# Kernel tuning notes

Measured on AMD Instinct MI355X. Metric: run time of the kernel, lower is better.

Reference implementation:

```python
import jax, jax.numpy as jnp
import numpy as np

N_NODES = 50000
N_EDGES = 800000
D_IN = 128
D_OUT = 128


def setup_inputs() -> dict:
    key = jax.random.key(0)
    k1, k2, k3, k4, k5 = jax.random.split(key, 5)
    x = jax.random.normal(k1, (N_NODES, D_IN), dtype=jnp.float32)
    edge_index = jax.random.randint(k2, (2, N_EDGES), 0, N_NODES, dtype=jnp.int64)
    scale = 1.0 / np.sqrt(D_IN)
    W_rel = jax.random.normal(k3, (D_OUT, D_IN), dtype=jnp.float32) * scale
    b_rel = jax.random.normal(k4, (D_OUT,), dtype=jnp.float32) * scale
    W_root = jax.random.normal(k5, (D_OUT, D_IN), dtype=jnp.float32) * scale
    return {"x": x, "edge_index": edge_index, "W_rel": W_rel, "b_rel": b_rel, "W_root": W_root}


def reference(x, edge_index, W_rel, b_rel, W_root):
    # PyG GraphConv (aggr='add'):
    #   out_i = W_rel @ (sum_{j->i} x_j) + b_rel + W_root @ x_i
    # followed by ReLU (normalization=None, dropout=0 -> identity).
    src = edge_index[0]  # message source j
    dst = edge_index[1]  # message target i
    n = x.shape[0]
    agg = jax.ops.segment_sum(x[src], dst, num_segments=n)  # [N, D_IN]
    out = agg @ W_rel.T + b_rel + x @ W_root.T              # [N, D_OUT]
    return jax.nn.relu(out)
```

## Files before the change

kernel.cpp:

```cpp
#include <hip/hip_runtime.h>
#include <hip/hip_bf16.h>


#define N_NODES 50000
#define N_EDGES 800000
#define D 128
#define SLOTS 40
#define CSTR 8
#define NPB 32
#define KC 32
#define SROW 136

#define CVT_N  (N_NODES * (D / 2))
#define PACK_N (8 * 8 * 64 * 8)
#define CNT_N  (N_NODES * CSTR + 4)

typedef __attribute__((ext_vector_type(8))) short short8;
typedef __attribute__((ext_vector_type(4))) float floatx4;

__device__ __forceinline__ float bf2f(unsigned short u) {
    return __uint_as_float((unsigned int)u << 16);
}
__device__ __forceinline__ unsigned short f2bf(float f) {
    __hip_bfloat16 h = __float2bfloat16(f);
    return *(unsigned short*)&h;
}

__device__ __forceinline__ int wave_detect_i64(const int* __restrict__ ei) {
    int lane = threadIdx.x & 63;
    int v = ei[2 * lane + 1];
    return __ballot(v == 0) == ~0ull;
}

__global__ __launch_bounds__(256) void zero_f4_kernel(float4* __restrict__ p, int n4) {
    int i = blockIdx.x * 256 + threadIdx.x;
    if (i < n4) p[i] = make_float4(0.f, 0.f, 0.f, 0.f);
}

__global__ void detect_kernel(const int* __restrict__ ei, int* __restrict__ flag) {
    if (threadIdx.x == 0 && blockIdx.x == 0) {
        int any = 0;
        for (int i = 0; i < 64; ++i) any |= ei[2 * i + 1];
        flag[0] = (any == 0) ? 1 : 0;
    }
}

__global__ __launch_bounds__(256) void prep_kernel(const float2* __restrict__ x2,
                                                   ushort2* __restrict__ xb2,
                                                   const float* __restrict__ Wrel,
                                                   const float* __restrict__ Wroot,
                                                   unsigned short* __restrict__ pwc,
                                                   int* __restrict__ cnt) {
    int i = blockIdx.x * 256 + threadIdx.x;
    if (i < CVT_N) {
        float2 f = x2[i];
        xb2[i] = make_ushort2(f2bf(f.x), f2bf(f.y));
    } else if (i < CVT_N + PACK_N) {
        int idx  = i - CVT_N;
        int j    = idx & 7;
        int lane = (idx >> 3) & 63;
        int n0   = (idx >> 9) & 7;
        int t    = idx >> 12;
        int n = n0 * 16 + (lane & 15);
        int k = t * 32 + (lane >> 4) * 8 + j;
        float w = (k < D) ? Wrel[n * D + k] : Wroot[n * D + (k - D)];
        pwc[idx] = f2bf(w);
    } else if (i < CVT_N + PACK_N + CNT_N) {
        cnt[i - CVT_N - PACK_N] = 0;
    }
}

__global__ __launch_bounds__(256) void append_kernel(const int* __restrict__ ei,
                                                     int* __restrict__ cnt,
                                                     int* __restrict__ slots,
                                                     int* __restrict__ ovf_cnt,
                                                     int* __restrict__ ovf) {
    int i64 = wave_detect_i64(ei);
    int base = (blockIdx.x * 256 + threadIdx.x) * 2;
    if (base >= N_EDGES) return;
    int s0, s1, d0, d1;
    if (i64) {
        int4 a = *(const int4*)&ei[2 * base];
        s0 = a.x; s1 = a.z;
        int4 c = *(const int4*)&ei[2 * N_EDGES + 2 * base];
        d0 = c.x; d1 = c.z;
    } else {
        int2 sv = *(const int2*)&ei[base];
        int2 dv = *(const int2*)&ei[N_EDGES + base];
        s0 = sv.x; s1 = sv.y;
        d0 = dv.x; d1 = dv.y;
    }
    bool v0 = (unsigned)s0 < N_NODES && (unsigned)d0 < N_NODES;
    bool v1 = (unsigned)s1 < N_NODES && (unsigned)d1 < N_NODES;
    int p0 = v0 ? atomicAdd(&cnt[d0 * CSTR], 1) : 0;
    int p1 = v1 ? atomicAdd(&cnt[d1 * CSTR], 1) : 0;
    if (v0) { if (p0 < SLOTS) slots[d0 * SLOTS + p0] = s0;
              else { int o = atomicAdd(ovf_cnt, 1); ovf[2 * o] = d0; ovf[2 * o + 1] = s0; } }
    if (v1) { if (p1 < SLOTS) slots[d1 * SLOTS + p1] = s1;
              else { int o = atomicAdd(ovf_cnt, 1); ovf[2 * o] = d1; ovf[2 * o + 1] = s1; } }
}

__global__ __launch_bounds__(256) void GraphConvLayer_55783035240593_kernel(
        const ushort2* __restrict__ xb2,
        const unsigned short* __restrict__ xb,
        const int* __restrict__ cnt,
        const int* __restrict__ slots,
        const int* __restrict__ ovf_cnt,
        const int* __restrict__ ovf,
        const unsigned short* __restrict__ pwc,
        const float* __restrict__ b_rel,
        float* __restrict__ out) {
    __shared__ unsigned short sA[16 * SROW];
    int wid  = threadIdx.x >> 6;
    int lane = threadIdx.x & 63;
    int node0 = blockIdx.x * 16;
    int tov = ovf_cnt[0];

    for (int li = 0; li < 4; ++li) {
        int node = node0 + wid * 4 + li;
        int kk = cnt[node * CSTR];
        if (kk > SLOTS) kk = SLOTS;
        int myidx = (lane < kk) ? slots[node * SLOTS + lane] : 0;
        float ax = 0.f, ay = 0.f;
        for (int j = 0; j < kk; j += 8) {
            int s0 = __shfl(myidx, j);
            int s1 = __shfl(myidx, j + 1);
            int s2 = __shfl(myidx, j + 2);
            int s3 = __shfl(myidx, j + 3);
            int s4 = __shfl(myidx, j + 4);
            int s5 = __shfl(myidx, j + 5);
            int s6 = __shfl(myidx, j + 6);
            int s7 = __shfl(myidx, j + 7);
            ushort2 u0 = xb2[(size_t)s0 * (D / 2) + lane];
            ushort2 u1 = xb2[(size_t)s1 * (D / 2) + lane];
            ushort2 u2 = xb2[(size_t)s2 * (D / 2) + lane];
            ushort2 u3 = xb2[(size_t)s3 * (D / 2) + lane];
            ushort2 u4 = xb2[(size_t)s4 * (D / 2) + lane];
            ushort2 u5 = xb2[(size_t)s5 * (D / 2) + lane];
            ushort2 u6 = xb2[(size_t)s6 * (D / 2) + lane];
            ushort2 u7 = xb2[(size_t)s7 * (D / 2) + lane];
            float m1 = (j + 1 < kk) ? 1.f : 0.f;
            float m2 = (j + 2 < kk) ? 1.f : 0.f;
            float m3 = (j + 3 < kk) ? 1.f : 0.f;
            float m4 = (j + 4 < kk) ? 1.f : 0.f;
            float m5 = (j + 5 < kk) ? 1.f : 0.f;
            float m6 = (j + 6 < kk) ? 1.f : 0.f;
            float m7 = (j + 7 < kk) ? 1.f : 0.f;
            ax += bf2f(u0.x) + m1 * bf2f(u1.x) + m2 * bf2f(u2.x) + m3 * bf2f(u3.x)
                + m4 * bf2f(u4.x) + m5 * bf2f(u5.x) + m6 * bf2f(u6.x) + m7 * bf2f(u7.x);
            ay += bf2f(u0.y) + m1 * bf2f(u1.y) + m2 * bf2f(u2.y) + m3 * bf2f(u3.y)
                + m4 * bf2f(u4.y) + m5 * bf2f(u5.y) + m6 * bf2f(u6.y) + m7 * bf2f(u7.y);
        }
        if (tov > 0) {
            for (int t2 = 0; t2 < tov; ++t2) {
                if (ovf[2 * t2] == node) {
                    ushort2 u = xb2[(size_t)ovf[2 * t2 + 1] * (D / 2) + lane];
                    ax += bf2f(u.x);
                    ay += bf2f(u.y);
                }
            }
        }
        *(ushort2*)&sA[(wid * 4 + li) * SROW + 2 * lane] =
            make_ushort2(f2bf(ax), f2bf(ay));
    }
    __syncthreads();

    int m = lane & 15, quad = lane >> 4;
    const unsigned short* arow = &sA[m * SROW + quad * 8];
    const unsigned short* xrow = xb + (size_t)(node0 + m) * D + quad * 8;

    floatx4 acc0 = (floatx4){0.f, 0.f, 0.f, 0.f};
    floatx4 acc1 = (floatx4){0.f, 0.f, 0.f, 0.f};
#pragma unroll
    for (int t = 0; t < 8; ++t) {
        short8 afrag = (t < 4) ? *(const short8*)(arow + t * 32)
                               : *(const short8*)(xrow + (t - 4) * 32);
        const unsigned short* bb = pwc + ((size_t)(t * 8 + wid * 2) * 64 + lane) * 8;
        short8 b0 = *(const short8*)bb;
        short8 b1 = *(const short8*)(bb + 64 * 8);
        acc0 = __builtin_amdgcn_mfma_f32_16x16x32_bf16(afrag, b0, acc0, 0, 0, 0);
        acc1 = __builtin_amdgcn_mfma_f32_16x16x32_bf16(afrag, b1, acc1, 0, 0, 0);
    }

#pragma unroll
    for (int q = 0; q < 2; ++q) {
        floatx4 a = q ? acc1 : acc0;
        int n = (wid * 2 + q) * 16 + m;
        float bias = b_rel[n];
#pragma unroll
        for (int r = 0; r < 4; ++r) {
            int node = node0 + quad * 4 + r;
            out[(size_t)node * D + n] = fmaxf(a[r] + bias, 0.f);
        }
    }
}

__global__ __launch_bounds__(256) void pack_w_kernel(const float* __restrict__ W,
                                                     float* __restrict__ pw) {
    int idx = blockIdx.x * 256 + threadIdx.x;
    if (idx >= D * D) return;
    int o = idx >> 7, k = idx & 127;
    pw[k * D + o] = W[o * D + k];
}

__global__ __launch_bounds__(256) void hist_kernel(const int* __restrict__ ei,
                                                   int* __restrict__ deg) {
    int i64 = wave_detect_i64(ei);
    int base = (blockIdx.x * 256 + threadIdx.x) * 4;
    if (base >= N_EDGES) return;
    int d0, d1, d2, d3;
    if (i64) {
        int4 a = *(const int4*)&ei[2 * N_EDGES + 2 * base];
        int4 b = *(const int4*)&ei[2 * N_EDGES + 2 * base + 4];
        d0 = a.x; d1 = a.z; d2 = b.x; d3 = b.z;
    } else {
        int4 v = *(const int4*)&ei[N_EDGES + base];
        d0 = v.x; d1 = v.y; d2 = v.z; d3 = v.w;
    }
    if ((unsigned)d0 < N_NODES) atomicAdd(&deg[d0], 1);
    if ((unsigned)d1 < N_NODES) atomicAdd(&deg[d1], 1);
    if ((unsigned)d2 < N_NODES) atomicAdd(&deg[d2], 1);
    if ((unsigned)d3 < N_NODES) atomicAdd(&deg[d3], 1);
}

__device__ __forceinline__ int wave_iscan(int v, int lane) {
#pragma unroll
    for (int off = 1; off < 64; off <<= 1) {
        int u = __shfl_up(v, off, 64);
        if (lane >= off) v += u;
    }
    return v;
}

__global__ __launch_bounds__(1024) void scan_kernel(const int* __restrict__ deg,
                                                    int* __restrict__ offsets,
                                                    int* __restrict__ cursor) {
    __shared__ int wsum[16];
    __shared__ int base_s;
    int t = threadIdx.x, lane = t & 63, w = t >> 6;
    if (t == 0) { base_s = 0; offsets[0] = 0; }
    __syncthreads();
    for (int c0 = 0; c0 < N_NODES; c0 += 1024) {
        int idx = c0 + t;
        int v = (idx < N_NODES) ? deg[idx] : 0;
        int inc = wave_iscan(v, lane);
        if (lane == 63) wsum[w] = inc;
        __syncthreads();
        if (w == 0) {
            int s = (lane < 16) ? wsum[lane] : 0;
            int si = wave_iscan(s, lane);
            if (lane < 16) wsum[lane] = si - s;
        }
        __syncthreads();
        int tot = base_s + wsum[w] + inc;
        if (idx < N_NODES) {
            offsets[idx + 1] = tot;
            cursor[idx] = tot - v;
        }
        __syncthreads();
        if (t == 1023) base_s = tot;
        __syncthreads();
    }
}

__global__ __launch_bounds__(256) void reorder_kernel(const int* __restrict__ ei,
                                                      int* __restrict__ cursor,
                                                      int* __restrict__ csr_src) {
    int i64 = wave_detect_i64(ei);
    int base = (blockIdx.x * 256 + threadIdx.x) * 4;
    if (base >= N_EDGES) return;
    int s0, s1, s2, s3, d0, d1, d2, d3;
    if (i64) {
        int4 a = *(const int4*)&ei[2 * base];
        int4 b = *(const int4*)&ei[2 * base + 4];
        s0 = a.x; s1 = a.z; s2 = b.x; s3 = b.z;
        int4 c = *(const int4*)&ei[2 * N_EDGES + 2 * base];
        int4 e = *(const int4*)&ei[2 * N_EDGES + 2 * base + 4];
        d0 = c.x; d1 = c.z; d2 = e.x; d3 = e.z;
    } else {
        int4 sv = *(const int4*)&ei[base];
        int4 dv = *(const int4*)&ei[N_EDGES + base];
        s0 = sv.x; s1 = sv.y; s2 = sv.z; s3 = sv.w;
        d0 = dv.x; d1 = dv.y; d2 = dv.z; d3 = dv.w;
    }
    bool v0 = (unsigned)s0 < N_NODES && (unsigned)d0 < N_NODES;
    bool v1 = (unsigned)s1 < N_NODES && (unsigned)d1 < N_NODES;
    bool v2 = (unsigned)s2 < N_NODES && (unsigned)d2 < N_NODES;
    bool v3 = (unsigned)s3 < N_NODES && (unsigned)d3 < N_NODES;
    int p0 = v0 ? atomicAdd(&cursor[d0], 1) : 0;
    int p1 = v1 ? atomicAdd(&cursor[d1], 1) : 0;
    int p2 = v2 ? atomicAdd(&cursor[d2], 1) : 0;
    int p3 = v3 ? atomicAdd(&cursor[d3], 1) : 0;
    if (v0) csr_src[p0] = s0;
    if (v1) csr_src[p1] = s1;
    if (v2) csr_src[p2] = s2;
    if (v3) csr_src[p3] = s3;
}

__global__ __launch_bounds__(256) void gather_kernel(const float2* __restrict__ x2,
                                                     const int* __restrict__ csr_src,
                                                     const int* __restrict__ offsets,
                                                     float2* __restrict__ agg2) {
    int node = blockIdx.x * 4 + (threadIdx.x >> 6);
    int lane = threadIdx.x & 63;
    if (node >= N_NODES) return;
    int beg = offsets[node], end = offsets[node + 1];
    float2 acc = make_float2(0.f, 0.f);
    for (int e = beg; e < end; ++e) {
        int s = csr_src[e];
        float2 f = x2[(size_t)s * (D / 2) + lane];
        acc.x += f.x;
        acc.y += f.y;
    }
    agg2[(size_t)node * (D / 2) + lane] = acc;
}

__global__ __launch_bounds__(256) void scatter_kernel(const float2* __restrict__ x2,
                                                      const int* __restrict__ ei,
                                                      const int* __restrict__ flag,
                                                      float* __restrict__ agg) {
    int wave = threadIdx.x >> 6;
    int lane = threadIdx.x & 63;
    int e = blockIdx.x * 4 + wave;
    if (e >= N_EDGES) return;
    int i64 = flag ? flag[0] : 0;
    int s, d;
    if (i64) { s = ei[2 * e]; d = ei[2 * N_EDGES + 2 * e]; }
    else     { s = ei[e];     d = ei[N_EDGES + e]; }
    if ((unsigned)s >= N_NODES || (unsigned)d >= N_NODES) return;
    float2 f = x2[(size_t)s * (D / 2) + lane];
    atomicAdd(&agg[(size_t)d * D + 2 * lane + 0], f.x);
    atomicAdd(&agg[(size_t)d * D + 2 * lane + 1], f.y);
}

__global__ __launch_bounds__(256) void gemm_f32_kernel(
        const float2* __restrict__ x2,
        const float* __restrict__ pwrel,
        const float* __restrict__ pwroot,
        const float* __restrict__ b_rel,
        float* __restrict__ out) {
    __shared__ float sWrel[KC * D];
    __shared__ float sWroot[KC * D];
    __shared__ float2 sAm[NPB * (KC / 2)];
    __shared__ float2 sXm[NPB * (KC / 2)];

    int t = threadIdx.x;
    int node0 = blockIdx.x * NPB;
    int tn = t >> 5;
    int to = t & 31;

    float acc[4][4];
#pragma unroll
    for (int a = 0; a < 4; ++a)
#pragma unroll
        for (int b = 0; b < 4; ++b) acc[a][b] = 0.0f;

    for (int c = 0; c < 4; ++c) {
        __syncthreads();
#pragma unroll
        for (int r = 0; r < 4; ++r) {
            int i = r * 256 + t;
            ((float4*)sWrel)[i]  = ((const float4*)(pwrel  + c * KC * D))[i];
            ((float4*)sWroot)[i] = ((const float4*)(pwroot + c * KC * D))[i];
        }
#pragma unroll
        for (int r = 0; r < 2; ++r) {
            int i = r * 256 + t;
            int n = i >> 4, k2 = i & 15;
            int node = node0 + n;
            float2 av = make_float2(0.f, 0.f), xv = make_float2(0.f, 0.f);
            if (node < N_NODES) {
                av = ((const float2*)out)[(size_t)node * (D / 2) + c * (KC / 2) + k2];
                xv = x2[(size_t)node * (D / 2) + c * (KC / 2) + k2];
            }
            sAm[i] = av;
            sXm[i] = xv;
        }
        __syncthreads();

#pragma unroll
        for (int k2 = 0; k2 < KC / 2; ++k2) {
            float4 wr0 = *(const float4*)&sWrel[(2 * k2 + 0) * D + to * 4];
            float4 wr1 = *(const float4*)&sWrel[(2 * k2 + 1) * D + to * 4];
            float4 wt0 = *(const float4*)&sWroot[(2 * k2 + 0) * D + to * 4];
            float4 wt1 = *(const float4*)&sWroot[(2 * k2 + 1) * D + to * 4];
#pragma unroll
            for (int ni = 0; ni < 4; ++ni) {
                float2 a  = sAm[(tn * 4 + ni) * (KC / 2) + k2];
                float2 xx = sXm[(tn * 4 + ni) * (KC / 2) + k2];
                acc[ni][0] += a.x * wr0.x + a.y * wr1.x + xx.x * wt0.x + xx.y * wt1.x;
                acc[ni][1] += a.x * wr0.y + a.y * wr1.y + xx.x * wt0.y + xx.y * wt1.y;
                acc[ni][2] += a.x * wr0.z + a.y * wr1.z + xx.x * wt0.z + xx.y * wt1.z;
                acc[ni][3] += a.x * wr0.w + a.y * wr1.w + xx.x * wt0.w + xx.y * wt1.w;
            }
        }
    }

    int o0 = to * 4;
    float4 bias = *(const float4*)&b_rel[o0];
#pragma unroll
    for (int ni = 0; ni < 4; ++ni) {
        int node = node0 + tn * 4 + ni;
        if (node >= N_NODES) continue;
        float4 v;
        v.x = fmaxf(acc[ni][0] + bias.x, 0.f);
        v.y = fmaxf(acc[ni][1] + bias.y, 0.f);
        v.z = fmaxf(acc[ni][2] + bias.z, 0.f);
        v.w = fmaxf(acc[ni][3] + bias.w, 0.f);
        *(float4*)&out[(size_t)node * D + o0] = v;
    }
}

__global__ __launch_bounds__(128) void gemm_fallback_kernel(const float* __restrict__ x,
                                                            const float* __restrict__ Wrel,
                                                            const float* __restrict__ Wroot,
                                                            const float* __restrict__ b_rel,
                                                            float* __restrict__ out) {
    __shared__ float rowA[D];
    __shared__ float rowX[D];
    int node = blockIdx.x;
    int o = threadIdx.x;
    rowA[o] = out[(size_t)node * D + o];
    rowX[o] = x[(size_t)node * D + o];
    __syncthreads();
    float acc = b_rel[o];
    const float4* wr = (const float4*)&Wrel[o * D];
    const float4* wt = (const float4*)&Wroot[o * D];
#pragma unroll 8
    for (int k4 = 0; k4 < D / 4; ++k4) {
        float4 w = wr[k4], u = wt[k4];
        const float* a = &rowA[k4 * 4];
        const float* xx = &rowX[k4 * 4];
        acc += a[0] * w.x + a[1] * w.y + a[2] * w.z + a[3] * w.w
             + xx[0] * u.x + xx[1] * u.y + xx[2] * u.z + xx[3] * u.w;
    }
    __syncthreads();
    out[(size_t)node * D + o] = fmaxf(acc, 0.f);
}

extern "C" void kernel_launch(void* const* d_in, const int* in_sizes, int n_in,
                              void* d_out, int out_size, void* d_ws, size_t ws_size,
                              hipStream_t stream) {
    const float* x      = (const float*)d_in[0];
    const int*   ei     = (const int*)d_in[1];
    const float* W_rel  = (const float*)d_in[2];
    const float* b_rel  = (const float*)d_in[3];
    const float* W_root = (const float*)d_in[4];
    float*       out    = (float*)d_out;

    char* p = (char*)d_ws;
    size_t o0 = 16;
    int*            flag    = (int*)p;
    unsigned short* pwc     = (unsigned short*)(p + o0);  o0 += (size_t)PACK_N * 2;
    unsigned short* xb      = (unsigned short*)(p + o0);  o0 += (size_t)N_NODES * D * 2;
    int*            cnt     = (int*)(p + o0);             o0 += (size_t)N_NODES * CSTR * 4;
    int*            ovf_cnt = (int*)(p + o0);             o0 += 16;
    int*            slots   = (int*)(p + o0);             o0 += (size_t)N_NODES * SLOTS * 4;
    int*            ovf     = (int*)(p + o0);             o0 += (size_t)N_EDGES * 8;
    const size_t need_full = o0;

    size_t m0 = 16;
    float* m_pwrel  = (float*)(p + m0);  m0 += (size_t)D * D * 4;
    float* m_pwroot = (float*)(p + m0);  m0 += (size_t)D * D * 4;
    int*   m_deg    = (int*)(p + m0);    m0 += (size_t)N_NODES * 4;
    int*   m_offs   = (int*)(p + m0);    m0 += ((size_t)N_NODES + 1) * 4 + 12;
    m0 &= ~15ull;
    int*   m_csr    = (int*)(p + m0);    m0 += (size_t)N_EDGES * 4;
    const size_t need_mid = m0;
    const size_t need_pw  = 16 + 2 * (size_t)D * D * 4;

    const int eb4 = (N_EDGES / 4 + 255) / 256;
    const int eb2 = (N_EDGES / 2 + 255) / 256;

    if (ws_size >= need_full) {
        const int prep_total = CVT_N + PACK_N + CNT_N;
        prep_kernel<<<(prep_total + 255) / 256, 256, 0, stream>>>(
            (const float2*)x, (ushort2*)xb, W_rel, W_root, pwc, cnt);
        append_kernel<<<eb2, 256, 0, stream>>>(ei, cnt, slots,
                                               cnt + N_NODES * CSTR, ovf);
        GraphConvLayer_55783035240593_kernel<<<N_NODES / 16, 256, 0, stream>>>(
            (const ushort2*)xb, xb, cnt, slots, cnt + N_NODES * CSTR, ovf,
            pwc, b_rel, out);
        (void)ovf_cnt;
    } else if (ws_size >= need_mid) {
        pack_w_kernel<<<64, 256, 0, stream>>>(W_rel, m_pwrel);
        pack_w_kernel<<<64, 256, 0, stream>>>(W_root, m_pwroot);
        zero_f4_kernel<<<(N_NODES / 4 + 255) / 256, 256, 0, stream>>>((float4*)m_deg,
                                                                      N_NODES / 4);
        hist_kernel<<<eb4, 256, 0, stream>>>(ei, m_deg);
        scan_kernel<<<1, 1024, 0, stream>>>(m_deg, m_offs, m_deg);
        reorder_kernel<<<eb4, 256, 0, stream>>>(ei, m_deg, m_csr);
        gather_kernel<<<N_NODES / 4, 256, 0, stream>>>((const float2*)x, m_csr,
                                                       m_offs, (float2*)out);
        gemm_f32_kernel<<<(N_NODES + NPB - 1) / NPB, 256, 0, stream>>>(
            (const float2*)x, m_pwrel, m_pwroot, b_rel, out);
    } else {
        bool have_flag = ws_size >= 16;
        bool have_pw   = ws_size >= need_pw;
        if (have_flag) detect_kernel<<<1, 64, 0, stream>>>(ei, flag);
        if (have_pw) {
            pack_w_kernel<<<64, 256, 0, stream>>>(W_rel, m_pwrel);
            pack_w_kernel<<<64, 256, 0, stream>>>(W_root, m_pwroot);
        }
        int n4 = N_NODES * D / 4;
        zero_f4_kernel<<<(n4 + 255) / 256, 256, 0, stream>>>((float4*)out, n4);
        scatter_kernel<<<N_EDGES / 4, 256, 0, stream>>>((const float2*)x, ei,
                                                        have_flag ? flag : nullptr, out);
        if (have_pw)
            gemm_f32_kernel<<<(N_NODES + NPB - 1) / NPB, 256, 0, stream>>>(
                (const float2*)x, m_pwrel, m_pwroot, b_rel, out);
        else
            gemm_fallback_kernel<<<N_NODES, 128, 0, stream>>>(x, W_rel, W_root, b_rel, out);
    }
}
```

Before: 177.2 us.

## Fuse prep, edge append and aggregation-GEMM into one persistent kernel with grid barriers

Replaces the three separate launches (prep/convert, edge append, gather+MFMA GEMM) with a single persistent kernel of 1024 blocks that uses software grid barriers between phases. It also packs the per-node counter into the slot row itself (stride 48, 47 slots plus count) and uses nontemporal stores. The intent is to cut launch overhead and inter-kernel gaps and to improve locality between count and slots. The risk is barrier spin cost, a deadlock if all 1024 blocks cannot be co-resident, and lower parallelism in the final phase because tiles are strided across a fixed grid.

Result: slower. 481.9 us (+171.9%).

```diff
diff --git a/kernel.cpp b/kernel.cpp
--- a/kernel.cpp
+++ b/kernel.cpp
@@ -5,15 +5,18 @@
 #define N_NODES 50000
 #define N_EDGES 800000
 #define D 128
-#define SLOTS 40
-#define CSTR 8
+#define NBLK 1024
+#define NTH (NBLK * 256)
+#define SLOT_STRIDE 48
+#define SLOT_CAP 47
+#define SROW 136
 #define NPB 32
 #define KC 32
-#define SROW 136
-
+
+#define EAPP   (N_EDGES / 2)
 #define CVT_N  (N_NODES * (D / 2))
 #define PACK_N (8 * 8 * 64 * 8)
-#define CNT_N  (N_NODES * CSTR + 4)
+#define PACK2_N (PACK_N / 2)
 
 typedef __attribute__((ext_vector_type(8))) short short8;
 typedef __attribute__((ext_vector_type(4))) float floatx4;
@@ -30,6 +33,191 @@
     int lane = threadIdx.x & 63;
     int v = ei[2 * lane + 1];
     return __ballot(v == 0) == ~0ull;
+}
+
+__device__ __forceinline__ void grid_barrier(int* bar, int target) {
+    __syncthreads();
+    if (threadIdx.x == 0) {
+        __threadfence();
+        atomicAdd(bar, 1);
+        while (atomicAdd(bar, 0) < target) __builtin_amdgcn_s_sleep(8);
+    }
+    __syncthreads();
+    __threadfence();
+}
+
+__global__ void init_ctl_kernel(int* __restrict__ ctl) {
+    if (threadIdx.x < 4) ctl[threadIdx.x] = 0;
+}
+
+__global__ __launch_bounds__(256, 4) void GraphConvLayer_55783035240593_kernel(
+        const float2* __restrict__ x2,
+        const int* __restrict__ ei,
+        const float* __restrict__ Wrel,
+        const float* __restrict__ Wroot,
+        const float* __restrict__ b_rel,
+        unsigned short* __restrict__ pwc,
+        unsigned short* __restrict__ xb,
+        int* __restrict__ slots,
+        int* __restrict__ ovf,
+        int* __restrict__ ctl,
+        float* __restrict__ out) {
+    __shared__ unsigned short sA[16 * SROW];
+    int tid  = threadIdx.x;
+    int gid  = blockIdx.x * 256 + tid;
+    int lane = tid & 63;
+    int wid  = tid >> 6;
+    int i64  = wave_detect_i64(ei);
+
+    for (int n = gid; n < N_NODES; n += NTH)
+        __builtin_nontemporal_store(0, &slots[n * SLOT_STRIDE]);
+
+    grid_barrier(ctl, NBLK);
+
+    const int total1 = EAPP + CVT_N + PACK2_N;
+    for (int i = gid; i < total1; i += NTH) {
+        if (i < EAPP) {
+            int base = i * 2;
+            int s0, s1, d0, d1;
+            if (i64) {
+                int4 a = *(const int4*)&ei[2 * base];
+                s0 = a.x; s1 = a.z;
+                int4 c = *(const int4*)&ei[2 * N_EDGES + 2 * base];
+                d0 = c.x; d1 = c.z;
+            } else {
+                int2 sv = *(const int2*)&ei[base];
+                int2 dv = *(const int2*)&ei[N_EDGES + base];
+                s0 = sv.x; s1 = sv.y;
+                d0 = dv.x; d1 = dv.y;
+            }
+            bool v0 = (unsigned)s0 < N_NODES && (unsigned)d0 < N_NODES;
+            bool v1 = (unsigned)s1 < N_NODES && (unsigned)d1 < N_NODES;
+            int p0 = v0 ? atomicAdd(&slots[d0 * SLOT_STRIDE], 1) : 0;
+            int p1 = v1 ? atomicAdd(&slots[d1 * SLOT_STRIDE], 1) : 0;
+            if (v0) {
+                if (p0 < SLOT_CAP)
+                    __builtin_nontemporal_store(s0, &slots[d0 * SLOT_STRIDE + 1 + p0]);
+                else {
+                    int o = atomicAdd(&ctl[1], 1);
+                    __builtin_nontemporal_store(d0, &ovf[2 * o]);
+                    __builtin_nontemporal_store(s0, &ovf[2 * o + 1]);
+                }
+            }
+            if (v1) {
+                if (p1 < SLOT_CAP)
+                    __builtin_nontemporal_store(s1, &slots[d1 * SLOT_STRIDE + 1 + p1]);
+                else {
+                    int o = atomicAdd(&ctl[1], 1);
+                    __builtin_nontemporal_store(d1, &ovf[2 * o]);
+                    __builtin_nontemporal_store(s1, &ovf[2 * o + 1]);
+                }
+            }
+        } else if (i < EAPP + CVT_N) {
+            int c = i - EAPP;
+            float2 f = x2[c];
+            unsigned int v = (unsigned int)f2bf(f.x) | ((unsigned int)f2bf(f.y) << 16);
+            __builtin_nontemporal_store(v, (unsigned int*)xb + c);
+        } else {
+            int pi = i - EAPP - CVT_N;
+            int idx  = 2 * pi;
+            int j    = idx & 7;
+            int ln   = (idx >> 3) & 63;
+            int n0   = (idx >> 9) & 7;
+            int t    = idx >> 12;
+            int n = n0 * 16 + (ln & 15);
+            int k = t * 32 + (ln >> 4) * 8 + j;
+            float w0 = (k     < D) ? Wrel[n * D + k]     : Wroot[n * D + (k - D)];
+            float w1 = (k + 1 < D) ? Wrel[n * D + k + 1] : Wroot[n * D + (k + 1 - D)];
+            unsigned int v = (unsigned int)f2bf(w0) | ((unsigned int)f2bf(w1) << 16);
+            __builtin_nontemporal_store(v, (unsigned int*)pwc + pi);
+        }
+    }
+
+    grid_barrier(ctl, 2 * NBLK);
+
+    int tov = ctl[1];
+    int m = lane & 15, quad = lane >> 4;
+
+    for (int tile = blockIdx.x; tile < N_NODES / 16; tile += NBLK) {
+        int node0 = tile * 16;
+
+        for (int li = 0; li < 4; ++li) {
+            int node = node0 + wid * 4 + li;
+            int kk = slots[node * SLOT_STRIDE];
+            if (kk > SLOT_CAP) kk = SLOT_CAP;
+            int myidx = (lane < kk) ? slots[node * SLOT_STRIDE + 1 + lane] : 0;
+            float ax = 0.f, ay = 0.f;
+            const ushort2* xb2 = (const ushort2*)xb;
+            for (int j = 0; j < kk; j += 8) {
+                int s0 = __shfl(myidx, j);
+                int s1 = __shfl(myidx, j + 1);
+                int s2 = __shfl(myidx, j + 2);
+                int s3 = __shfl(myidx, j + 3);
+                int s4 = __shfl(myidx, j + 4);
+                int s5 = __shfl(myidx, j + 5);
+                int s6 = __shfl(myidx, j + 6);
+                int s7 = __shfl(myidx, j + 7);
+                ushort2 u0 = xb2[(size_t)s0 * (D / 2) + lane];
+                ushort2 u1 = xb2[(size_t)s1 * (D / 2) + lane];
+                ushort2 u2 = xb2[(size_t)s2 * (D / 2) + lane];
+                ushort2 u3 = xb2[(size_t)s3 * (D / 2) + lane];
+                ushort2 u4 = xb2[(size_t)s4 * (D / 2) + lane];
+                ushort2 u5 = xb2[(size_t)s5 * (D / 2) + lane];
+                ushort2 u6 = xb2[(size_t)s6 * (D / 2) + lane];
+                ushort2 u7 = xb2[(size_t)s7 * (D / 2) + lane];
+                float m1 = (j + 1 < kk) ? 1.f : 0.f;
+                float m2 = (j + 2 < kk) ? 1.f : 0.f;
+                float m3 = (j + 3 < kk) ? 1.f : 0.f;
+                float m4 = (j + 4 < kk) ? 1.f : 0.f;
+                float m5 = (j + 5 < kk) ? 1.f : 0.f;
+                float m6 = (j + 6 < kk) ? 1.f : 0.f;
+                float m7 = (j + 7 < kk) ? 1.f : 0.f;
+                ax += bf2f(u0.x) + m1 * bf2f(u1.x) + m2 * bf2f(u2.x) + m3 * bf2f(u3.x)
+                    + m4 * bf2f(u4.x) + m5 * bf2f(u5.x) + m6 * bf2f(u6.x) + m7 * bf2f(u7.x);
+                ay += bf2f(u0.y) + m1 * bf2f(u1.y) + m2 * bf2f(u2.y) + m3 * bf2f(u3.y)
+                    + m4 * bf2f(u4.y) + m5 * bf2f(u5.y) + m6 * bf2f(u6.y) + m7 * bf2f(u7.y);
+            }
+            if (tov > 0) {
+                for (int t2 = 0; t2 < tov; ++t2) {
+                    if (ovf[2 * t2] == node) {
+                        ushort2 u = xb2[(size_t)ovf[2 * t2 + 1] * (D / 2) + lane];
+                        ax += bf2f(u.x);
+                        ay += bf2f(u.y);
+                    }
+                }
+            }
+            *(ushort2*)&sA[(wid * 4 + li) * SROW + 2 * lane] =
+                make_ushort2(f2bf(ax), f2bf(ay));
+        }
+        __syncthreads();
+
+        const unsigned short* arow = &sA[m * SROW + quad * 8];
+        const unsigned short* xrow = xb + (size_t)(node0 + m) * D + quad * 8;
+        floatx4 acc0 = (floatx4){0.f, 0.f, 0.f, 0.f};
+        floatx4 acc1 = (floatx4){0.f, 0.f, 0.f, 0.f};
+#pragma unroll
+        for (int t = 0; t < 8; ++t) {
+            short8 afrag = (t < 4) ? *(const short8*)(arow + t * 32)
+                                   : *(const short8*)(xrow + (t - 4) * 32);
+            const unsigned short* bb = pwc + ((size_t)(t * 8 + wid * 2) * 64 + lane) * 8;
+            short8 b0 = *(const short8*)bb;
+            short8 b1 = *(const short8*)(bb + 64 * 8);
+            acc0 = __builtin_amdgcn_mfma_f32_16x16x32_bf16(afrag, b0, acc0, 0, 0, 0);
+            acc1 = __builtin_amdgcn_mfma_f32_16x16x32_bf16(afrag, b1, acc1, 0, 0, 0);
+        }
+#pragma unroll
+        for (int q = 0; q < 2; ++q) {
+            floatx4 a = q ? acc1 : acc0;
+            int n = (wid * 2 + q) * 16 + m;
+            float bias = b_rel[n];
+#pragma unroll
+            for (int r = 0; r < 4; ++r) {
+                int node = node0 + quad * 4 + r;
+                out[(size_t)node * D + n] = fmaxf(a[r] + bias, 0.f);
+            }
+        }
+        __syncthreads();
+    }
 }
 
 __global__ __launch_bounds__(256) void zero_f4_kernel(float4* __restrict__ p, int n4) {
@@ -42,156 +230,6 @@
         int any = 0;
         for (int i = 0; i < 64; ++i) any |= ei[2 * i + 1];
         flag[0] = (any == 0) ? 1 : 0;
-    }
-}
-
-__global__ __launch_bounds__(256) void prep_kernel(const float2* __restrict__ x2,
-                                                   ushort2* __restrict__ xb2,
-                                                   const float* __restrict__ Wrel,
-                                                   const float* __restrict__ Wroot,
-                                                   unsigned short* __restrict__ pwc,
-                                                   int* __restrict__ cnt) {
-    int i = blockIdx.x * 256 + threadIdx.x;
-    if (i < CVT_N) {
-        float2 f = x2[i];
-        xb2[i] = make_ushort2(f2bf(f.x), f2bf(f.y));
-    } else if (i < CVT_N + PACK_N) {
-        int idx  = i - CVT_N;
-        int j    = idx & 7;
-        int lane = (idx >> 3) & 63;
-        int n0   = (idx >> 9) & 7;
-        int t    = idx >> 12;
-        int n = n0 * 16 + (lane & 15);
-        int k = t * 32 + (lane >> 4) * 8 + j;
-        float w = (k < D) ? Wrel[n * D + k] : Wroot[n * D + (k - D)];
-        pwc[idx] = f2bf(w);
-    } else if (i < CVT_N + PACK_N + CNT_N) {
-        cnt[i - CVT_N - PACK_N] = 0;
-    }
-}
-
-__global__ __launch_bounds__(256) void append_kernel(const int* __restrict__ ei,
-                                                     int* __restrict__ cnt,
-                                                     int* __restrict__ slots,
-                                                     int* __restrict__ ovf_cnt,
-                                                     int* __restrict__ ovf) {
-    int i64 = wave_detect_i64(ei);
-    int base = (blockIdx.x * 256 + threadIdx.x) * 2;
-    if (base >= N_EDGES) return;
-    int s0, s1, d0, d1;
-    if (i64) {
-        int4 a = *(const int4*)&ei[2 * base];
-        s0 = a.x; s1 = a.z;
-        int4 c = *(const int4*)&ei[2 * N_EDGES + 2 * base];
-        d0 = c.x; d1 = c.z;
-    } else {
-        int2 sv = *(const int2*)&ei[base];
-        int2 dv = *(const int2*)&ei[N_EDGES + base];
-        s0 = sv.x; s1 = sv.y;
-        d0 = dv.x; d1 = dv.y;
-    }
-    bool v0 = (unsigned)s0 < N_NODES && (unsigned)d0 < N_NODES;
-    bool v1 = (unsigned)s1 < N_NODES && (unsigned)d1 < N_NODES;
-    int p0 = v0 ? atomicAdd(&cnt[d0 * CSTR], 1) : 0;
-    int p1 = v1 ? atomicAdd(&cnt[d1 * CSTR], 1) : 0;
-    if (v0) { if (p0 < SLOTS) slots[d0 * SLOTS + p0] = s0;
-              else { int o = atomicAdd(ovf_cnt, 1); ovf[2 * o] = d0; ovf[2 * o + 1] = s0; } }
-    if (v1) { if (p1 < SLOTS) slots[d1 * SLOTS + p1] = s1;
-              else { int o = atomicAdd(ovf_cnt, 1); ovf[2 * o] = d1; ovf[2 * o + 1] = s1; } }
-}
-
-__global__ __launch_bounds__(256) void GraphConvLayer_55783035240593_kernel(
-        const ushort2* __restrict__ xb2,
-        const unsigned short* __restrict__ xb,
-        const int* __restrict__ cnt,
-        const int* __restrict__ slots,
-        const int* __restrict__ ovf_cnt,
-        const int* __restrict__ ovf,
-        const unsigned short* __restrict__ pwc,
-        const float* __restrict__ b_rel,
-        float* __restrict__ out) {
-    __shared__ unsigned short sA[16 * SROW];
-    int wid  = threadIdx.x >> 6;
-    int lane = threadIdx.x & 63;
-    int node0 = blockIdx.x * 16;
-    int tov = ovf_cnt[0];
-
-    for (int li = 0; li < 4; ++li) {
-        int node = node0 + wid * 4 + li;
-        int kk = cnt[node * CSTR];
-        if (kk > SLOTS) kk = SLOTS;
-        int myidx = (lane < kk) ? slots[node * SLOTS + lane] : 0;
-        float ax = 0.f, ay = 0.f;
-        for (int j = 0; j < kk; j += 8) {
-            int s0 = __shfl(myidx, j);
-            int s1 = __shfl(myidx, j + 1);
-            int s2 = __shfl(myidx, j + 2);
-            int s3 = __shfl(myidx, j + 3);
-            int s4 = __shfl(myidx, j + 4);
-            int s5 = __shfl(myidx, j + 5);
-            int s6 = __shfl(myidx, j + 6);
-            int s7 = __shfl(myidx, j + 7);
-            ushort2 u0 = xb2[(size_t)s0 * (D / 2) + lane];
-            ushort2 u1 = xb2[(size_t)s1 * (D / 2) + lane];
-            ushort2 u2 = xb2[(size_t)s2 * (D / 2) + lane];
-            ushort2 u3 = xb2[(size_t)s3 * (D / 2) + lane];
-            ushort2 u4 = xb2[(size_t)s4 * (D / 2) + lane];
-            ushort2 u5 = xb2[(size_t)s5 * (D / 2) + lane];
-            ushort2 u6 = xb2[(size_t)s6 * (D / 2) + lane];
-            ushort2 u7 = xb2[(size_t)s7 * (D / 2) + lane];
-            float m1 = (j + 1 < kk) ? 1.f : 0.f;
-            float m2 = (j + 2 < kk) ? 1.f : 0.f;
-            float m3 = (j + 3 < kk) ? 1.f : 0.f;
-            float m4 = (j + 4 < kk) ? 1.f : 0.f;
-            float m5 = (j + 5 < kk) ? 1.f : 0.f;
-            float m6 = (j + 6 < kk) ? 1.f : 0.f;
-            float m7 = (j + 7 < kk) ? 1.f : 0.f;
-            ax += bf2f(u0.x) + m1 * bf2f(u1.x) + m2 * bf2f(u2.x) + m3 * bf2f(u3.x)
-                + m4 * bf2f(u4.x) + m5 * bf2f(u5.x) + m6 * bf2f(u6.x) + m7 * bf2f(u7.x);
-            ay += bf2f(u0.y) + m1 * bf2f(u1.y) + m2 * bf2f(u2.y) + m3 * bf2f(u3.y)
-                + m4 * bf2f(u4.y) + m5 * bf2f(u5.y) + m6 * bf2f(u6.y) + m7 * bf2f(u7.y);
-        }
-        if (tov > 0) {
-            for (int t2 = 0; t2 < tov; ++t2) {
-                if (ovf[2 * t2] == node) {
-                    ushort2 u = xb2[(size_t)ovf[2 * t2 + 1] * (D / 2) + lane];
-                    ax += bf2f(u.x);
-                    ay += bf2f(u.y);
-                }
-            }
-        }
-        *(ushort2*)&sA[(wid * 4 + li) * SROW + 2 * lane] =
-            make_ushort2(f2bf(ax), f2bf(ay));
-    }
-    __syncthreads();
-
-    int m = lane & 15, quad = lane >> 4;
-    const unsigned short* arow = &sA[m * SROW + quad * 8];
-    const unsigned short* xrow = xb + (size_t)(node0 + m) * D + quad * 8;
-
-    floatx4 acc0 = (floatx4){0.f, 0.f, 0.f, 0.f};
-    floatx4 acc1 = (floatx4){0.f, 0.f, 0.f, 0.f};
-#pragma unroll
-    for (int t = 0; t < 8; ++t) {
-        short8 afrag = (t < 4) ? *(const short8*)(arow + t * 32)
-                               : *(const short8*)(xrow + (t - 4) * 32);
-        const unsigned short* bb = pwc + ((size_t)(t * 8 + wid * 2) * 64 + lane) * 8;
-        short8 b0 = *(const short8*)bb;
-        short8 b1 = *(const short8*)(bb + 64 * 8);
-        acc0 = __builtin_amdgcn_mfma_f32_16x16x32_bf16(afrag, b0, acc0, 0, 0, 0);
-        acc1 = __builtin_amdgcn_mfma_f32_16x16x32_bf16(afrag, b1, acc1, 0, 0, 0);
-    }
-
-#pragma unroll
-    for (int q = 0; q < 2; ++q) {
-        floatx4 a = q ? acc1 : acc0;
-        int n = (wid * 2 + q) * 16 + m;
-        float bias = b_rel[n];
-#pragma unroll
-        for (int r = 0; r < 4; ++r) {
-            int node = node0 + quad * 4 + r;
-            out[(size_t)node * D + n] = fmaxf(a[r] + bias, 0.f);
-        }
     }
 }
 
@@ -343,18 +381,14 @@
     __shared__ float sWroot[KC * D];
     __shared__ float2 sAm[NPB * (KC / 2)];
     __shared__ float2 sXm[NPB * (KC / 2)];
-
     int t = threadIdx.x;
     int node0 = blockIdx.x * NPB;
-    int tn = t >> 5;
-    int to = t & 31;
-
+    int tn = t >> 5, to = t & 31;
     float acc[4][4];
 #pragma unroll
     for (int a = 0; a < 4; ++a)
 #pragma unroll
         for (int b = 0; b < 4; ++b) acc[a][b] = 0.0f;
-
     for (int c = 0; c < 4; ++c) {
         __syncthreads();
 #pragma unroll
@@ -377,7 +411,6 @@
             sXm[i] = xv;
         }
         __syncthreads();
-
 #pragma unroll
         for (int k2 = 0; k2 < KC / 2; ++k2) {
             float4 wr0 = *(const float4*)&sWrel[(2 * k2 + 0) * D + to * 4];
@@ -395,7 +428,6 @@
             }
         }
     }
-
     int o0 = to * 4;
     float4 bias = *(const float4*)&b_rel[o0];
 #pragma unroll
@@ -450,16 +482,15 @@
 
     char* p = (char*)d_ws;
     size_t o0 = 16;
-    int*            flag    = (int*)p;
-    unsigned short* pwc     = (unsigned short*)(p + o0);  o0 += (size_t)PACK_N * 2;
-    unsigned short* xb      = (unsigned short*)(p + o0);  o0 += (size_t)N_NODES * D * 2;
-    int*            cnt     = (int*)(p + o0);             o0 += (size_t)N_NODES * CSTR * 4;
-    int*            ovf_cnt = (int*)(p + o0);             o0 += 16;
-    int*            slots   = (int*)(p + o0);             o0 += (size_t)N_NODES * SLOTS * 4;
-    int*            ovf     = (int*)(p + o0);             o0 += (size_t)N_EDGES * 8;
+    int*            ctl   = (int*)p;
+    unsigned short* pwc   = (unsigned short*)(p + o0);  o0 += (size_t)PACK_N * 2;
+    unsigned short* xb    = (unsigned short*)(p + o0);  o0 += (size_t)N_NODES * D * 2;
+    int*            slots = (int*)(p + o0);             o0 += (size_t)N_NODES * SLOT_STRIDE * 4;
+    int*            ovf   = (int*)(p + o0);             o0 += (size_t)N_EDGES * 8;
     const size_t need_full = o0;
 
     size_t m0 = 16;
+    int*   flag     = (int*)p;
     float* m_pwrel  = (float*)(p + m0);  m0 += (size_t)D * D * 4;
     float* m_pwroot = (float*)(p + m0);  m0 += (size_t)D * D * 4;
     int*   m_deg    = (int*)(p + m0);    m0 += (size_t)N_NODES * 4;
@@ -470,18 +501,11 @@
     const size_t need_pw  = 16 + 2 * (size_t)D * D * 4;
 
     const int eb4 = (N_EDGES / 4 + 255) / 256;
-    const int eb2 = (N_EDGES / 2 + 255) / 256;
 
     if (ws_size >= need_full) {
-        const int prep_total = CVT_N + PACK_N + CNT_N;
-        prep_kernel<<<(prep_total + 255) / 256, 256, 0, stream>>>(
-            (const float2*)x, (ushort2*)xb, W_rel, W_root, pwc, cnt);
-        append_kernel<<<eb2, 256, 0, stream>>>(ei, cnt, slots,
-                                               cnt + N_NODES * CSTR, ovf);
-        GraphConvLayer_55783035240593_kernel<<<N_NODES / 16, 256, 0, stream>>>(
-            (const ushort2*)xb, xb, cnt, slots, cnt + N_NODES * CSTR, ovf,
-            pwc, b_rel, out);
-        (void)ovf_cnt;
+        init_ctl_kernel<<<1, 64, 0, stream>>>(ctl);
+        GraphConvLayer_55783035240593_kernel<<<NBLK, 256, 0, stream>>>(
+            (const float2*)x, ei, W_rel, W_root, b_rel, pwc, xb, slots, ovf, ctl, out);
     } else if (ws_size >= need_mid) {
         pack_w_kernel<<<64, 256, 0, stream>>>(W_rel, m_pwrel);
         pack_w_kernel<<<64, 256, 0, stream>>>(W_root, m_pwroot);
```
